# Kernel optimization log

Hardware: AMD Instinct MI355X
Metric: run time of the kernel (lower is better)

The kernel has to match this reference:

```python
import jax, jax.numpy as jnp
import numpy as np

B, N, DIM = 8, 4096, 512
HEADS, DHEAD = 8, 64
HIDDEN = HEADS * DHEAD  # 512
COND = 512
EPS = 1e-5


def layer_norm(x, gamma, beta):
    mu = jnp.mean(x, axis=-1, keepdims=True)
    var = jnp.var(x, axis=-1, keepdims=True)
    return (x - mu) * jax.lax.rsqrt(var + EPS) * gamma + beta


def setup_inputs() -> dict:
    key = jax.random.key(0)
    ks = jax.random.split(key, 8)
    s_in = 1.0 / np.sqrt(DIM)
    s_cond = 1.0 / np.sqrt(COND)
    s_hid = 1.0 / np.sqrt(HIDDEN)
    return {
        "x": jax.random.normal(ks[0], (B, N, DIM), jnp.float32),
        "conditioning_embeddings": jax.random.normal(ks[1], (B, COND), jnp.float32),
        "gamma_in": jnp.ones((DIM,), jnp.float32),
        "w_cond": jax.random.normal(ks[2], (2 * DIM, COND), jnp.float32) * s_cond,
        "b_cond": jax.random.normal(ks[3], (2 * DIM,), jnp.float32) * 0.01,
        "w_qkv": jax.random.normal(ks[4], (3 * HIDDEN, DIM), jnp.float32) * s_in,
        "w_out": jax.random.normal(ks[5], (DIM, HIDDEN), jnp.float32) * s_hid,
        "gamma_out": jnp.ones((DIM,), jnp.float32),
    }


def reference(x, conditioning_embeddings, gamma_in, w_cond, b_cond, w_qkv, w_out, gamma_out):
    scale_f = DHEAD ** (-0.5)
    # pre-norm
    x = layer_norm(x, gamma_in, jnp.zeros_like(gamma_in))
    # conditioning affine: SiLU -> Linear -> broadcast over tokens
    cond = jax.nn.silu(conditioning_embeddings) @ w_cond.T + b_cond  # [b, 2*dim]
    scale, shift = jnp.split(cond, 2, axis=-1)
    x = x * (scale[:, None, :] + 1.0) + shift[:, None, :]
    # qkv projection (no bias)
    qkv = x @ w_qkv.T  # [b, n, 3*hidden]
    q, k, v = jnp.split(qkv, 3, axis=-1)
    def to_heads(t):
        return t.reshape(B, N, HEADS, DHEAD).transpose(0, 2, 1, 3)  # b h n d
    q, k, v = to_heads(q), to_heads(k), to_heads(v)
    q = jax.nn.softmax(q, axis=-1) * scale_f  # softmax over feature dim
    k = jax.nn.softmax(k, axis=-2)            # softmax over sequence dim
    context = jnp.einsum('bhnd,bhne->bhde', k, v)
    out = jnp.einsum('bhde,bhnd->bhne', context, q)
    out = out.transpose(0, 2, 1, 3).reshape(B, N, HIDDEN)  # b n (h d)
    out = out @ w_out.T
    return layer_norm(out, gamma_out, jnp.zeros_like(gamma_out))
```

## Files before the change

### kernel.cpp

```cpp
#include <hip/hip_runtime.h>
#include <hip/hip_bf16.h>
#include <math.h>

typedef unsigned short u16;
typedef __attribute__((ext_vector_type(4))) float f32x4;
typedef __attribute__((ext_vector_type(8))) short s16x8;

#define B_    8
#define N_    4096
#define DIM_  512
#define TOK   32768
#define QKVD  1536

__device__ __forceinline__ float bf2f(u16 u) {
    union { unsigned int i; float f; } x; x.i = ((unsigned int)u) << 16; return x.f;
}
__device__ __forceinline__ u16 f2bf(float f) {
    union { float f; unsigned int i; } x; x.f = f;
    unsigned int r = (x.i + 0x7fffu + ((x.i >> 16) & 1u)) >> 16;
    return (u16)r;
}

__device__ __forceinline__ void gload_lds16(const void* g, void* l) {
    __builtin_amdgcn_global_load_lds(
        (const __attribute__((address_space(1))) unsigned int*)g,
        (__attribute__((address_space(3))) unsigned int*)l, 16, 0, 0);
}

__device__ __forceinline__ int swz8(int row, int p) { return p ^ (row & 7); }

__global__ void k_cond(const float* __restrict__ ce, const float* __restrict__ w_cond,
                       const float* __restrict__ b_cond, float* __restrict__ cond)
{
    __shared__ float s[512];
    int jt = blockIdx.x, b = blockIdx.y;
    int tid = threadIdx.x, wid = tid >> 6, lane = tid & 63;
    for (int i = tid; i < 512; i += 256) {
        float v = ce[b * 512 + i];
        s[i] = v / (1.f + __expf(-v));
    }
    __syncthreads();
#pragma unroll
    for (int jj = 0; jj < 4; ++jj) {
        int j = jt * 16 + wid * 4 + jj;
        const float4* w4 = (const float4*)(w_cond + (size_t)j * 512);
        float4 a = w4[lane * 2], c = w4[lane * 2 + 1];
        float acc = a.x*s[lane*8+0] + a.y*s[lane*8+1] + a.z*s[lane*8+2] + a.w*s[lane*8+3]
                  + c.x*s[lane*8+4] + c.y*s[lane*8+5] + c.z*s[lane*8+6] + c.w*s[lane*8+7];
#pragma unroll
        for (int d = 1; d < 64; d <<= 1) acc += __shfl_xor(acc, d, 64);
        if (lane == 0) cond[b * 1024 + j] = acc + b_cond[j];
    }
}

__global__ void k_w2bf(const float* __restrict__ w, u16* __restrict__ wb)
{
    int i = (blockIdx.x * 256 + threadIdx.x) * 4;
    float4 v = *(const float4*)&w[i];
    ushort4 o; o.x = f2bf(v.x); o.y = f2bf(v.y); o.z = f2bf(v.z); o.w = f2bf(v.w);
    *(ushort4*)&wb[i] = o;
}

__global__ void k_lnmod(const float* __restrict__ x, const float* __restrict__ cond,
                        const float* __restrict__ gamma, u16* __restrict__ xm)
{
    int wave = threadIdx.x >> 6, lane = threadIdx.x & 63;
    size_t t = (size_t)blockIdx.x * 4 + wave;
    const float* xr = x + t * 512;
    float4 v0 = ((const float4*)xr)[lane * 2];
    float4 v1 = ((const float4*)xr)[lane * 2 + 1];
    float s  = v0.x+v0.y+v0.z+v0.w + v1.x+v1.y+v1.z+v1.w;
    float ss = v0.x*v0.x+v0.y*v0.y+v0.z*v0.z+v0.w*v0.w
             + v1.x*v1.x+v1.y*v1.y+v1.z*v1.z+v1.w*v1.w;
#pragma unroll
    for (int m = 1; m < 64; m <<= 1) { s += __shfl_xor(s, m, 64); ss += __shfl_xor(ss, m, 64); }
    float mu = s * (1.f/512.f);
    float var = ss * (1.f/512.f) - mu * mu;
    float rs = rsqrtf(var + 1e-5f);
    int b = (int)(t >> 12);
    const float* cb = cond + b * 1024;
    float4 g0  = ((const float4*)gamma)[lane*2],     g1  = ((const float4*)gamma)[lane*2+1];
    float4 sc0 = ((const float4*)cb)[lane*2],        sc1 = ((const float4*)cb)[lane*2+1];
    float4 sh0 = ((const float4*)(cb+512))[lane*2],  sh1 = ((const float4*)(cb+512))[lane*2+1];
    ushort4 o0, o1;
    o0.x = f2bf(((v0.x-mu)*rs*g0.x)*(1.f+sc0.x) + sh0.x);
    o0.y = f2bf(((v0.y-mu)*rs*g0.y)*(1.f+sc0.y) + sh0.y);
    o0.z = f2bf(((v0.z-mu)*rs*g0.z)*(1.f+sc0.z) + sh0.z);
    o0.w = f2bf(((v0.w-mu)*rs*g0.w)*(1.f+sc0.w) + sh0.w);
    o1.x = f2bf(((v1.x-mu)*rs*g1.x)*(1.f+sc1.x) + sh1.x);
    o1.y = f2bf(((v1.y-mu)*rs*g1.y)*(1.f+sc1.y) + sh1.y);
    o1.z = f2bf(((v1.z-mu)*rs*g1.z)*(1.f+sc1.z) + sh1.z);
    o1.w = f2bf(((v1.w-mu)*rs*g1.w)*(1.f+sc1.w) + sh1.w);
    ushort4* orow = (ushort4*)(xm + t * 512);
    orow[lane * 2] = o0; orow[lane * 2 + 1] = o1;
}

__global__ __launch_bounds__(256, 3)
void k_gemmqkv(const u16* __restrict__ A,
               const u16* __restrict__ Bm,
               u16* __restrict__ Out)
{
    __shared__ __align__(16) u16 As[128 * 64];
    __shared__ __align__(16) u16 Bs[128 * 64];
    int sid = (blockIdx.x & 7) * 384 + (blockIdx.x >> 3);
    int bn = sid % 12, bm = sid / 12;
    int m0 = bm * 128, n0 = bn * 128;
    int tid = threadIdx.x;
    int wid = tid >> 6, lane = tid & 63;
    int wr = (wid >> 1) * 64, wc = (wid & 1) * 64;
    int fr = lane & 15, fc = lane >> 4;

    f32x4 acc[4][4];
#pragma unroll
    for (int m = 0; m < 4; ++m)
#pragma unroll
        for (int n = 0; n < 4; ++n) acc[m][n] = (f32x4)0.f;

    for (int k0 = 0; k0 < 512; k0 += 64) {
#pragma unroll
        for (int i = 0; i < 4; ++i) {
            int c = tid + i * 256;
            int row = c >> 3, p = c & 7, gp = swz8(row, p);
            gload_lds16(A  + (size_t)(m0 + row) * 512 + k0 + gp * 8, &As[c * 8]);
            gload_lds16(Bm + (size_t)(n0 + row) * 512 + k0 + gp * 8, &Bs[c * 8]);
        }
        __syncthreads();
#pragma unroll
        for (int kk = 0; kk < 2; ++kk) {
            s16x8 af[4], bfr[4];
            int q = kk * 4 + fc;
#pragma unroll
            for (int m = 0; m < 4; ++m) {
                int row = wr + m * 16 + fr;
                af[m] = *(const s16x8*)&As[(row * 8 + swz8(row, q)) * 8];
            }
#pragma unroll
            for (int n = 0; n < 4; ++n) {
                int row = wc + n * 16 + fr;
                bfr[n] = *(const s16x8*)&Bs[(row * 8 + swz8(row, q)) * 8];
            }
#pragma unroll
            for (int m = 0; m < 4; ++m)
#pragma unroll
                for (int n = 0; n < 4; ++n)
                    acc[m][n] = __builtin_amdgcn_mfma_f32_16x16x32_bf16(af[m], bfr[n], acc[m][n], 0, 0, 0);
        }
        __syncthreads();
    }

    int rbase = m0 + wr + fc * 4;
    int cbase = n0 + wc + fr;

    if (bn < 4) {
#pragma unroll
        for (int m = 0; m < 4; ++m) {
            float v[4][4];
#pragma unroll
            for (int n = 0; n < 4; ++n)
#pragma unroll
                for (int r = 0; r < 4; ++r) v[n][r] = acc[m][n][r];
#pragma unroll
            for (int r = 0; r < 4; ++r) {
                float mx = fmaxf(fmaxf(v[0][r], v[1][r]), fmaxf(v[2][r], v[3][r]));
#pragma unroll
                for (int d = 1; d < 16; d <<= 1) mx = fmaxf(mx, __shfl_xor(mx, d, 64));
                float e0 = __expf(v[0][r]-mx), e1 = __expf(v[1][r]-mx);
                float e2 = __expf(v[2][r]-mx), e3 = __expf(v[3][r]-mx);
                float sm = e0 + e1 + e2 + e3;
#pragma unroll
                for (int d = 1; d < 16; d <<= 1) sm += __shfl_xor(sm, d, 64);
                float rv = 0.125f / sm;
                v[0][r] = e0*rv; v[1][r] = e1*rv; v[2][r] = e2*rv; v[3][r] = e3*rv;
            }
#pragma unroll
            for (int n = 0; n < 4; ++n)
#pragma unroll
                for (int r = 0; r < 4; ++r)
                    Out[(size_t)(rbase + m*16 + r) * QKVD + (cbase + n*16)] = f2bf(v[n][r]);
        }
    } else {
#pragma unroll
        for (int m = 0; m < 4; ++m)
#pragma unroll
            for (int n = 0; n < 4; ++n)
#pragma unroll
                for (int r = 0; r < 4; ++r)
                    Out[(size_t)(rbase + m*16 + r) * QKVD + (cbase + n*16)] = f2bf(acc[m][n][r]);
    }
}

__global__ __launch_bounds__(256, 2)
void k_ctx(const u16* __restrict__ qkv, float* __restrict__ ctxp, float* __restrict__ ksump)
{
    __shared__ __align__(16) u16 sA[4][64 * 40];
    __shared__ __align__(16) u16 sB[4][64 * 40];
    __shared__ float scr[2][4096];
    __shared__ float kscr[2][64];
    int nc = blockIdx.x, h = blockIdx.y, b = blockIdx.z;
    int wid = threadIdx.x >> 6, lane = threadIdx.x & 63;
    u16* A  = sA[wid];
    u16* Bt = sB[wid];
    int fr = lane & 15, fk = (lane >> 4) * 8;
    f32x4 acc[4][4];
#pragma unroll
    for (int m = 0; m < 4; ++m)
#pragma unroll
        for (int n = 0; n < 4; ++n) acc[m][n] = (f32x4)0.f;
    float ksl = 0.f;

    size_t rowbase = (size_t)b * 4096 + nc * 512 + wid * 32;
    const u16* kp = qkv + rowbase * QKVD + 512 + h * 64 + lane;
    const u16* vp = kp + 512;

    for (int it = 0; it < 4; ++it) {
        const u16* kq = kp + (size_t)it * 128 * QKVD;
        const u16* vq = vp + (size_t)it * 128 * QKVD;
        unsigned int pk[16], pv[16];
#pragma unroll
        for (int j = 0; j < 16; ++j) {
            float a0 = __expf(bf2f(kq[(size_t)(2*j)   * QKVD]));
            float a1 = __expf(bf2f(kq[(size_t)(2*j+1) * QKVD]));
            ksl += a0 + a1;
            pk[j] = (unsigned)f2bf(a0) | ((unsigned)f2bf(a1) << 16);
            float b0 = bf2f(vq[(size_t)(2*j)   * QKVD]);
            float b1 = bf2f(vq[(size_t)(2*j+1) * QKVD]);
            pv[j] = (unsigned)f2bf(b0) | ((unsigned)f2bf(b1) << 16);
        }
#pragma unroll
        for (int j = 0; j < 4; ++j) {
            *(uint4*)&A [lane * 40 + j * 8] = *(uint4*)&pk[j * 4];
            *(uint4*)&Bt[lane * 40 + j * 8] = *(uint4*)&pv[j * 4];
        }
        s16x8 af[4], bfr[4];
#pragma unroll
        for (int m = 0; m < 4; ++m) af[m]  = *(const s16x8*)&A [(m * 16 + fr) * 40 + fk];
#pragma unroll
        for (int n = 0; n < 4; ++n) bfr[n] = *(const s16x8*)&Bt[(n * 16 + fr) * 40 + fk];
#pragma unroll
        for (int m = 0; m < 4; ++m)
#pragma unroll
            for (int n = 0; n < 4; ++n)
                acc[m][n] = __builtin_amdgcn_mfma_f32_16x16x32_bf16(af[m], bfr[n], acc[m][n], 0, 0, 0);
    }

    __syncthreads();
    int rbase = (lane >> 4) * 4, cbase = lane & 15;
    if (wid >= 2) {
#pragma unroll
        for (int m = 0; m < 4; ++m)
#pragma unroll
            for (int n = 0; n < 4; ++n)
#pragma unroll
                for (int r = 0; r < 4; ++r)
                    scr[wid - 2][(m * 16 + rbase + r) * 64 + n * 16 + cbase] = acc[m][n][r];
        kscr[wid - 2][lane] = ksl;
    }
    __syncthreads();
    if (wid < 2) {
        float* cp = ctxp + (((size_t)(b * 8 + h) * 16) + nc * 2 + wid) * 4096;
#pragma unroll
        for (int m = 0; m < 4; ++m)
#pragma unroll
            for (int n = 0; n < 4; ++n)
#pragma unroll
                for (int r = 0; r < 4; ++r) {
                    int idx = (m * 16 + rbase + r) * 64 + n * 16 + cbase;
                    cp[idx] = acc[m][n][r] + scr[wid][idx];
                }
        ksump[(((size_t)(b * 8 + h) * 16) + nc * 2 + wid) * 64 + lane] = ksl + kscr[wid][lane];
    }
}

__global__ void k_csum(const float* __restrict__ ctxp, const float* __restrict__ ksump,
                       float* __restrict__ ctxs)
{
    __shared__ float inv[64];
    int h = blockIdx.x, b = blockIdx.y;
    int tid = threadIdx.x;
    const float* cp = ctxp + (size_t)(b * 8 + h) * 16 * 4096;
    const float* kp = ksump + (size_t)(b * 8 + h) * 16 * 64;
    if (tid < 64) {
        float s = 0.f;
#pragma unroll
        for (int sl = 0; sl < 16; ++sl) s += kp[sl * 64 + tid];
        inv[tid] = 1.f / s;
    }
    __syncthreads();
    float* op = ctxs + (size_t)(b * 8 + h) * 4096;
    for (int idx = tid; idx < 4096; idx += 256) {
        float sum = 0.f;
#pragma unroll
        for (int sl = 0; sl < 16; ++sl) sum += cp[sl * 4096 + idx];
        op[idx] = sum * inv[idx >> 6];
    }
}

__global__ void k_wc(const float* __restrict__ ctxs, const float* __restrict__ w_out,
                     u16* __restrict__ Wc)
{
    __shared__ float csh[64 * 65];
    __shared__ float wsh[64 * 65];
    int jt = blockIdx.x, h = blockIdx.y, b = blockIdx.z;
    int tid = threadIdx.x;
    const float* cp = ctxs + (size_t)(b * 8 + h) * 4096;
    for (int idx = tid; idx < 4096; idx += 256) {
        int d = idx >> 6, e = idx & 63;
        csh[d * 65 + e] = cp[idx];
        wsh[d * 65 + e] = w_out[(size_t)(jt * 64 + d) * 512 + h * 64 + e];
    }
    __syncthreads();
    int j0 = (tid >> 4) * 4, d0 = (tid & 15) * 4;
    float acc[4][4] = {};
    for (int e = 0; e < 64; ++e) {
        float wv[4], cv[4];
#pragma unroll
        for (int i = 0; i < 4; ++i) wv[i] = wsh[(j0 + i) * 65 + e];
#pragma unroll
        for (int j = 0; j < 4; ++j) cv[j] = csh[(d0 + j) * 65 + e];
#pragma unroll
        for (int i = 0; i < 4; ++i)
#pragma unroll
            for (int j = 0; j < 4; ++j) acc[i][j] += wv[i] * cv[j];
    }
#pragma unroll
    for (int i = 0; i < 4; ++i)
#pragma unroll
        for (int j = 0; j < 4; ++j)
            Wc[((size_t)b * 512 + jt * 64 + j0 + i) * 512 + h * 64 + d0 + j] = f2bf(acc[i][j]);
}

__global__ __launch_bounds__(512, 2)
void k_g2ln(const u16* __restrict__ Aq, const u16* __restrict__ Wc,
            const float* __restrict__ gamma, float* __restrict__ out)
{
    __shared__ __align__(16) u16 As[64 * 64];
    __shared__ __align__(16) u16 Bs[512 * 64];
    __shared__ float rsum[64][8], rssq[64][8];
    int bm = blockIdx.x;
    int m0 = bm * 64;
    int b = m0 >> 12;
    const u16* Bp = Wc + (size_t)b * 512 * 512;
    int tid = threadIdx.x;
    int wn = tid >> 6, lane = tid & 63;
    int fr = lane & 15, fc = lane >> 4;

    f32x4 acc[4][4];
#pragma unroll
    for (int m = 0; m < 4; ++m)
#pragma unroll
        for (int n = 0; n < 4; ++n) acc[m][n] = (f32x4)0.f;

    for (int k0 = 0; k0 < 512; k0 += 64) {
        {
            int c = tid;
            int row = c >> 3, p = c & 7, gp = swz8(row, p);
            gload_lds16(Aq + (size_t)(m0 + row) * QKVD + k0 + gp * 8, &As[c * 8]);
        }
#pragma unroll
        for (int i = 0; i < 8; ++i) {
            int c = tid + i * 512;
            int col = c >> 3, p = c & 7, gp = swz8(col, p);
            gload_lds16(Bp + (size_t)col * 512 + k0 + gp * 8, &Bs[c * 8]);
        }
        __syncthreads();
#pragma unroll
        for (int kk = 0; kk < 2; ++kk) {
            int q = kk * 4 + fc;
            s16x8 af[4], bfr[4];
#pragma unroll
            for (int m = 0; m < 4; ++m) {
                int row = m * 16 + fr;
                af[m] = *(const s16x8*)&As[(row * 8 + swz8(row, q)) * 8];
            }
#pragma unroll
            for (int n = 0; n < 4; ++n) {
                int col = wn * 64 + n * 16 + fr;
                bfr[n] = *(const s16x8*)&Bs[(col * 8 + swz8(col, q)) * 8];
            }
#pragma unroll
            for (int m = 0; m < 4; ++m)
#pragma unroll
                for (int n = 0; n < 4; ++n)
                    acc[m][n] = __builtin_amdgcn_mfma_f32_16x16x32_bf16(af[m], bfr[n], acc[m][n], 0, 0, 0);
        }
        __syncthreads();
    }

#pragma unroll
    for (int m = 0; m < 4; ++m)
#pragma unroll
        for (int r = 0; r < 4; ++r) {
            float s = 0.f, ss = 0.f;
#pragma unroll
            for (int n = 0; n < 4; ++n) { float v = acc[m][n][r]; s += v; ss += v * v; }
#pragma unroll
            for (int d = 1; d < 16; d <<= 1) { s += __shfl_xor(s, d, 64); ss += __shfl_xor(ss, d, 64); }
            if ((lane & 15) == 0) {
                int row = m * 16 + fc * 4 + r;
                rsum[row][wn] = s; rssq[row][wn] = ss;
            }
        }
    __syncthreads();

    float g[4];
#pragma unroll
    for (int n = 0; n < 4; ++n) g[n] = gamma[wn * 64 + n * 16 + fr];

#pragma unroll
    for (int m = 0; m < 4; ++m)
#pragma unroll
        for (int r = 0; r < 4; ++r) {
            int row = m * 16 + fc * 4 + r;
            float s  = 0.f, ss = 0.f;
#pragma unroll
            for (int w = 0; w < 8; ++w) { s += rsum[row][w]; ss += rssq[row][w]; }
            float mu = s * (1.f/512.f);
            float var = ss * (1.f/512.f) - mu * mu;
            float rs = rsqrtf(var + 1e-5f);
            float* orow = out + (size_t)(m0 + row) * 512;
#pragma unroll
            for (int n = 0; n < 4; ++n)
                orow[wn * 64 + n * 16 + fr] = (acc[m][n][r] - mu) * rs * g[n];
        }
}

extern "C" void kernel_launch(void* const* d_in, const int* in_sizes, int n_in,
                              void* d_out, int out_size, void* d_ws, size_t ws_size,
                              hipStream_t stream)
{
    const float* x        = (const float*)d_in[0];
    const float* ce       = (const float*)d_in[1];
    const float* gamma_in = (const float*)d_in[2];
    const float* w_cond   = (const float*)d_in[3];
    const float* b_cond   = (const float*)d_in[4];
    const float* w_qkv    = (const float*)d_in[5];
    const float* w_out    = (const float*)d_in[6];
    const float* gamma_out= (const float*)d_in[7];
    float* out = (float*)d_out;

    char* ws = (char*)d_ws;
    size_t o = 0;
    auto take = [&](size_t bytes) -> char* {
        char* p = ws + o; o += (bytes + 255) & ~(size_t)255; return p;
    };
    float* cond  = (float*)take(8 * 1024 * 4);
    u16*   wqkvb = (u16*)  take((size_t)1536 * 512 * 2);
    float* ksump = (float*)take((size_t)64 * 16 * 64 * 4);
    float* ctxp  = (float*)take((size_t)64 * 16 * 4096 * 4);
    float* ctxs  = (float*)take((size_t)64 * 4096 * 4);
    u16*   Wc    = (u16*)  take((size_t)8 * 512 * 512 * 2);
    u16*   xm    = (u16*)  take((size_t)TOK * 512 * 2);
    u16*   qkv   = (u16*)  take((size_t)TOK * QKVD * 2);

    k_cond   <<<dim3(64, 8), 256, 0, stream>>>(ce, w_cond, b_cond, cond);
    k_w2bf   <<<768, 256, 0, stream>>>(w_qkv, wqkvb);
    k_lnmod  <<<8192, 256, 0, stream>>>(x, cond, gamma_in, xm);
    k_gemmqkv<<<3072, 256, 0, stream>>>(xm, wqkvb, qkv);
    k_ctx    <<<dim3(8, 8, 8), 256, 0, stream>>>(qkv, ctxp, ksump);
    k_csum   <<<dim3(8, 8), 256, 0, stream>>>(ctxp, ksump, ctxs);
    k_wc     <<<dim3(8, 8, 8), 256, 0, stream>>>(ctxs, w_out, Wc);
    k_g2ln   <<<512, 512, 0, stream>>>(qkv, Wc, gamma_out, out);
}
```

Before: 165.6 us.

## Fuse key exp and transpose into QKV GEMM epilogue, simplify context kernel

```diff
diff --git a/kernel.cpp b/kernel.cpp
--- a/kernel.cpp
+++ b/kernel.cpp
@@ -98,7 +98,9 @@
 __global__ __launch_bounds__(256, 3)
 void k_gemmqkv(const u16* __restrict__ A,
                const u16* __restrict__ Bm,
-               u16* __restrict__ Out)
+               u16* __restrict__ qb,
+               u16* __restrict__ ekT, u16* __restrict__ vT,
+               float* __restrict__ psum)
 {
     __shared__ __align__(16) u16 As[128 * 64];
     __shared__ __align__(16) u16 Bs[128 * 64];
@@ -148,10 +150,12 @@
         __syncthreads();
     }
 
+    int bloc = m0 >> 12;
     int rbase = m0 + wr + fc * 4;
-    int cbase = n0 + wc + fr;
+    int nl0 = (m0 & 4095) + wr + fc * 4;
 
     if (bn < 4) {
+        int cbase = n0 + wc + fr;
 #pragma unroll
         for (int m = 0; m < 4; ++m) {
             float v[4][4];
@@ -176,66 +180,71 @@
             for (int n = 0; n < 4; ++n)
 #pragma unroll
                 for (int r = 0; r < 4; ++r)
-                    Out[(size_t)(rbase + m*16 + r) * QKVD + (cbase + n*16)] = f2bf(v[n][r]);
+                    qb[(size_t)(rbase + m*16 + r) * 512 + (cbase + n*16)] = f2bf(v[n][r]);
+        }
+    } else if (bn < 8) {
+        int rcc = ((m0 & 4095) + wr) >> 6;
+        u16* ek = ekT + (size_t)bloc * 512 * 4096;
+#pragma unroll
+        for (int n = 0; n < 4; ++n) {
+            int c = (n0 - 512) + wc + n * 16 + fr;
+            float sm = 0.f;
+#pragma unroll
+            for (int m = 0; m < 4; ++m) {
+                u16 u0 = f2bf(__expf(acc[m][n][0]));
+                u16 u1 = f2bf(__expf(acc[m][n][1]));
+                u16 u2 = f2bf(__expf(acc[m][n][2]));
+                u16 u3 = f2bf(__expf(acc[m][n][3]));
+                sm += bf2f(u0) + bf2f(u1) + bf2f(u2) + bf2f(u3);
+                ushort4 pk; pk.x = u0; pk.y = u1; pk.z = u2; pk.w = u3;
+                *(ushort4*)&ek[(size_t)c * 4096 + nl0 + m * 16] = pk;
+            }
+            sm += __shfl_xor(sm, 16, 64);
+            sm += __shfl_xor(sm, 32, 64);
+            if (lane < 16) psum[(bloc * 64 + rcc) * 512 + c] = sm;
         }
     } else {
-#pragma unroll
-        for (int m = 0; m < 4; ++m)
-#pragma unroll
-            for (int n = 0; n < 4; ++n)
-#pragma unroll
-                for (int r = 0; r < 4; ++r)
-                    Out[(size_t)(rbase + m*16 + r) * QKVD + (cbase + n*16)] = f2bf(acc[m][n][r]);
+        u16* vt = vT + (size_t)bloc * 512 * 4096;
+#pragma unroll
+        for (int n = 0; n < 4; ++n) {
+            int c = (n0 - 1024) + wc + n * 16 + fr;
+#pragma unroll
+            for (int m = 0; m < 4; ++m) {
+                ushort4 pv;
+                pv.x = f2bf(acc[m][n][0]); pv.y = f2bf(acc[m][n][1]);
+                pv.z = f2bf(acc[m][n][2]); pv.w = f2bf(acc[m][n][3]);
+                *(ushort4*)&vt[(size_t)c * 4096 + nl0 + m * 16] = pv;
+            }
+        }
     }
 }
 
 __global__ __launch_bounds__(256, 2)
-void k_ctx(const u16* __restrict__ qkv, float* __restrict__ ctxp, float* __restrict__ ksump)
-{
-    __shared__ __align__(16) u16 sA[4][64 * 40];
-    __shared__ __align__(16) u16 sB[4][64 * 40];
+void k_ctx2(const u16* __restrict__ ekT, const u16* __restrict__ vT,
+            float* __restrict__ ctxp)
+{
     __shared__ float scr[2][4096];
-    __shared__ float kscr[2][64];
-    int nc = blockIdx.x, h = blockIdx.y, b = blockIdx.z;
+    int sl = blockIdx.x, h = blockIdx.y, b = blockIdx.z;
     int wid = threadIdx.x >> 6, lane = threadIdx.x & 63;
-    u16* A  = sA[wid];
-    u16* Bt = sB[wid];
-    int fr = lane & 15, fk = (lane >> 4) * 8;
+    int fr = lane & 15, fc = lane >> 4;
+    const u16* ek = ekT + ((size_t)b * 512 + h * 64) * 4096;
+    const u16* vt = vT  + ((size_t)b * 512 + h * 64) * 4096;
+    int nb = sl * 512 + wid * 128;
+
     f32x4 acc[4][4];
 #pragma unroll
     for (int m = 0; m < 4; ++m)
 #pragma unroll
         for (int n = 0; n < 4; ++n) acc[m][n] = (f32x4)0.f;
-    float ksl = 0.f;
-
-    size_t rowbase = (size_t)b * 4096 + nc * 512 + wid * 32;
-    const u16* kp = qkv + rowbase * QKVD + 512 + h * 64 + lane;
-    const u16* vp = kp + 512;
-
-    for (int it = 0; it < 4; ++it) {
-        const u16* kq = kp + (size_t)it * 128 * QKVD;
-        const u16* vq = vp + (size_t)it * 128 * QKVD;
-        unsigned int pk[16], pv[16];
-#pragma unroll
-        for (int j = 0; j < 16; ++j) {
-            float a0 = __expf(bf2f(kq[(size_t)(2*j)   * QKVD]));
-            float a1 = __expf(bf2f(kq[(size_t)(2*j+1) * QKVD]));
-            ksl += a0 + a1;
-            pk[j] = (unsigned)f2bf(a0) | ((unsigned)f2bf(a1) << 16);
-            float b0 = bf2f(vq[(size_t)(2*j)   * QKVD]);
-            float b1 = bf2f(vq[(size_t)(2*j+1) * QKVD]);
-            pv[j] = (unsigned)f2bf(b0) | ((unsigned)f2bf(b1) << 16);
-        }
-#pragma unroll
-        for (int j = 0; j < 4; ++j) {
-            *(uint4*)&A [lane * 40 + j * 8] = *(uint4*)&pk[j * 4];
-            *(uint4*)&Bt[lane * 40 + j * 8] = *(uint4*)&pv[j * 4];
-        }
+
+#pragma unroll
+    for (int ks = 0; ks < 4; ++ks) {
+        int n0k = nb + ks * 32 + fc * 8;
         s16x8 af[4], bfr[4];
 #pragma unroll
-        for (int m = 0; m < 4; ++m) af[m]  = *(const s16x8*)&A [(m * 16 + fr) * 40 + fk];
-#pragma unroll
-        for (int n = 0; n < 4; ++n) bfr[n] = *(const s16x8*)&Bt[(n * 16 + fr) * 40 + fk];
+        for (int m = 0; m < 4; ++m) af[m]  = *(const s16x8*)&ek[(size_t)(m * 16 + fr) * 4096 + n0k];
+#pragma unroll
+        for (int n = 0; n < 4; ++n) bfr[n] = *(const s16x8*)&vt[(size_t)(n * 16 + fr) * 4096 + n0k];
 #pragma unroll
         for (int m = 0; m < 4; ++m)
 #pragma unroll
@@ -253,11 +262,10 @@
 #pragma unroll
                 for (int r = 0; r < 4; ++r)
                     scr[wid - 2][(m * 16 + rbase + r) * 64 + n * 16 + cbase] = acc[m][n][r];
-        kscr[wid - 2][lane] = ksl;
     }
     __syncthreads();
     if (wid < 2) {
-        float* cp = ctxp + (((size_t)(b * 8 + h) * 16) + nc * 2 + wid) * 4096;
+        float* cp = ctxp + (((size_t)(b * 8 + h) * 16) + sl * 2 + wid) * 4096;
 #pragma unroll
         for (int m = 0; m < 4; ++m)
 #pragma unroll
@@ -267,22 +275,20 @@
                     int idx = (m * 16 + rbase + r) * 64 + n * 16 + cbase;
                     cp[idx] = acc[m][n][r] + scr[wid][idx];
                 }
-        ksump[(((size_t)(b * 8 + h) * 16) + nc * 2 + wid) * 64 + lane] = ksl + kscr[wid][lane];
-    }
-}
-
-__global__ void k_csum(const float* __restrict__ ctxp, const float* __restrict__ ksump,
+    }
+}
+
+__global__ void k_csum(const float* __restrict__ ctxp, const float* __restrict__ psum,
                        float* __restrict__ ctxs)
 {
     __shared__ float inv[64];
     int h = blockIdx.x, b = blockIdx.y;
     int tid = threadIdx.x;
     const float* cp = ctxp + (size_t)(b * 8 + h) * 16 * 4096;
-    const float* kp = ksump + (size_t)(b * 8 + h) * 16 * 64;
     if (tid < 64) {
         float s = 0.f;
 #pragma unroll
-        for (int sl = 0; sl < 16; ++sl) s += kp[sl * 64 + tid];
+        for (int ch = 0; ch < 64; ++ch) s += psum[(b * 64 + ch) * 512 + h * 64 + tid];
         inv[tid] = 1.f / s;
     }
     __syncthreads();
@@ -354,7 +360,7 @@
         {
             int c = tid;
             int row = c >> 3, p = c & 7, gp = swz8(row, p);
-            gload_lds16(Aq + (size_t)(m0 + row) * QKVD + k0 + gp * 8, &As[c * 8]);
+            gload_lds16(Aq + (size_t)(m0 + row) * 512 + k0 + gp * 8, &As[c * 8]);
         }
 #pragma unroll
         for (int i = 0; i < 8; ++i) {
@@ -445,19 +451,21 @@
     };
     float* cond  = (float*)take(8 * 1024 * 4);
     u16*   wqkvb = (u16*)  take((size_t)1536 * 512 * 2);
-    float* ksump = (float*)take((size_t)64 * 16 * 64 * 4);
+    float* psum  = (float*)take((size_t)8 * 64 * 512 * 4);
     float* ctxp  = (float*)take((size_t)64 * 16 * 4096 * 4);
     float* ctxs  = (float*)take((size_t)64 * 4096 * 4);
     u16*   Wc    = (u16*)  take((size_t)8 * 512 * 512 * 2);
     u16*   xm    = (u16*)  take((size_t)TOK * 512 * 2);
-    u16*   qkv   = (u16*)  take((size_t)TOK * QKVD * 2);
+    u16*   qb    = (u16*)  take((size_t)TOK * 512 * 2);
+    u16*   ekT   = (u16*)  take((size_t)B_ * 512 * 4096 * 2);
+    u16*   vT    = (u16*)  take((size_t)B_ * 512 * 4096 * 2);
 
     k_cond   <<<dim3(64, 8), 256, 0, stream>>>(ce, w_cond, b_cond, cond);
     k_w2bf   <<<768, 256, 0, stream>>>(w_qkv, wqkvb);
     k_lnmod  <<<8192, 256, 0, stream>>>(x, cond, gamma_in, xm);
-    k_gemmqkv<<<3072, 256, 0, stream>>>(xm, wqkvb, qkv);
-    k_ctx    <<<dim3(8, 8, 8), 256, 0, stream>>>(qkv, ctxp, ksump);
-    k_csum   <<<dim3(8, 8), 256, 0, stream>>>(ctxp, ksump, ctxs);
+    k_gemmqkv<<<3072, 256, 0, stream>>>(xm, wqkvb, qb, ekT, vT, psum);
+    k_ctx2   <<<dim3(8, 8, 8), 256, 0, stream>>>(ekT, vT, ctxp);
+    k_csum   <<<dim3(8, 8), 256, 0, stream>>>(ctxp, psum, ctxs);
     k_wc     <<<dim3(8, 8, 8), 256, 0, stream>>>(ctxs, w_out, Wc);
-    k_g2ln   <<<512, 512, 0, stream>>>(qkv, Wc, gamma_out, out);
-}
+    k_g2ln   <<<512, 512, 0, stream>>>(qb, Wc, gamma_out, out);
+}
```

New measurement: 176.8 us. +6.8%, slower.
